# Kernel tuning notes

Measured on AMD Instinct MI355X. Metric: run time of the kernel, lower is better.

The kernel has to match this reference:

```python
import jax, jax.numpy as jnp
import numpy as np


def setup_inputs() -> dict:
    key = jax.random.key(0)
    kq, kk, kv = jax.random.split(key, 3)
    B, S, D = 4, 4096, 64
    return {
        "q": jax.random.normal(kq, (B, S, D), dtype=jnp.float32),
        "k": jax.random.normal(kk, (B, S, D), dtype=jnp.float32),
        "v": jax.random.normal(kv, (B, S, D), dtype=jnp.float32),
    }


def reference(q, k, v):
    B, S, D = q.shape
    scale = 1.0 / jnp.sqrt(jnp.asarray(D, dtype=q.dtype))
    # (B, S, S) full score matrix, as in the naive torch implementation
    scores = jnp.einsum("bqd,bkd->bqk", q, k) * scale
    causal_mask = jnp.tril(jnp.ones((S, S), dtype=bool))  # True = keep
    scores = jnp.where(causal_mask, scores, -jnp.inf)
    attn = jax.nn.softmax(scores, axis=-1)
    return jnp.einsum("bqk,bkd->bqd", attn, v)
```

## Files before the change

### kernel.cpp

```cpp
#include <hip/hip_runtime.h>
#include <hip/hip_bf16.h>

typedef __bf16 bf16x8 __attribute__((ext_vector_type(8)));
typedef __bf16 bf16x4 __attribute__((ext_vector_type(4)));
typedef float  floatx4 __attribute__((ext_vector_type(4)));

#define SD 4096
#define DH 64
#define NB 4

__device__ __forceinline__ float exp2fast(float x) { return __builtin_amdgcn_exp2f(x); }

__device__ __forceinline__ unsigned pack_bf16_2(float a, float b) {
    union { __bf16 h[2]; unsigned u; } cvt;
    cvt.h[0] = (__bf16)a; cvt.h[1] = (__bf16)b;
    return cvt.u;
}

__device__ __forceinline__ void sync_all() {
    asm volatile("s_waitcnt vmcnt(0) lgkmcnt(0)\n\ts_barrier" ::: "memory");
}

__device__ __forceinline__ void load_lds16(const void* g, void* l) {
    __builtin_amdgcn_global_load_lds(
        (const __attribute__((address_space(1))) unsigned int*)g,
        (__attribute__((address_space(3))) unsigned int*)l, 16, 0, 0);
}

__device__ __forceinline__ int swz8(int g) {
    int row = g >> 3, ch = g & 7;
    return row * 64 + ((ch ^ (row & 7)) << 3);
}

__global__ __launch_bounds__(256) void prep_kernel(const float* __restrict__ k,
                                                   const float* __restrict__ v,
                                                   __bf16* __restrict__ kbs,
                                                   __bf16* __restrict__ vts) {
    __shared__ __bf16 tile[64][72];
    const int bid = blockIdx.x;
    const int tid = threadIdx.x;
    const long base = (long)bid * 4096;

    {
        const float* src = k + base + tid * 16;
        float4 f0 = *(const float4*)(src);
        float4 f1 = *(const float4*)(src + 4);
        float4 f2 = *(const float4*)(src + 8);
        float4 f3 = *(const float4*)(src + 12);
        bf16x8 c0, c1;
        c0[0]=(__bf16)f0.x; c0[1]=(__bf16)f0.y; c0[2]=(__bf16)f0.z; c0[3]=(__bf16)f0.w;
        c0[4]=(__bf16)f1.x; c0[5]=(__bf16)f1.y; c0[6]=(__bf16)f1.z; c0[7]=(__bf16)f1.w;
        c1[0]=(__bf16)f2.x; c1[1]=(__bf16)f2.y; c1[2]=(__bf16)f2.z; c1[3]=(__bf16)f2.w;
        c1[4]=(__bf16)f3.x; c1[5]=(__bf16)f3.y; c1[6]=(__bf16)f3.z; c1[7]=(__bf16)f3.w;
        __bf16* dst = kbs + base;
        *(bf16x8*)(dst + swz8(tid * 2))     = c0;
        *(bf16x8*)(dst + swz8(tid * 2 + 1)) = c1;
    }
    {
        int r = tid >> 2, ds0 = (tid & 3) * 16;
#pragma unroll
        for (int i = 0; i < 4; ++i) {
            float4 f = *(const float4*)(v + base + r * 64 + ds0 + i * 4);
            tile[ds0 + i*4 + 0][r] = (__bf16)f.x;
            tile[ds0 + i*4 + 1][r] = (__bf16)f.y;
            tile[ds0 + i*4 + 2][r] = (__bf16)f.z;
            tile[ds0 + i*4 + 3][r] = (__bf16)f.w;
        }
    }
    __syncthreads();
    {
        __bf16* dst = vts + base;
#pragma unroll
        for (int h = 0; h < 2; ++h) {
            int qc = tid * 2 + h;
            int d = qc >> 3, c8 = (qc & 7) * 8;
            bf16x8 o;
#pragma unroll
            for (int i = 0; i < 8; ++i) {
                int col = c8 + i;
                int key = ((col >> 5) * 2 + ((col >> 2) & 1)) * 16
                        + ((col >> 3) & 3) * 4 + (col & 3);
                o[i] = tile[d][key];
            }
            *(bf16x8*)(dst + swz8(qc)) = o;
        }
    }
}

__global__ __launch_bounds__(256, 4) void fa_kernel(const float* __restrict__ q,
                                                    const __bf16* __restrict__ kbs,
                                                    const __bf16* __restrict__ vts,
                                                    __bf16* __restrict__ opart,
                                                    float* __restrict__ lpart) {
    __shared__ __bf16 smem[2][8192];

    const int tid  = threadIdx.x;
    const int wave = tid >> 6;
    const int lane = tid & 63;
    const int c    = lane & 15;
    const int quad = lane >> 4;
    const int bid   = blockIdx.x;
    const int batch = bid & 3;
    const int pr    = (bid >> 2) & 31;
    const int qr    = bid >> 7;
    const float sc = 0.125f * 1.4426950408889634f;

    const long offB = (long)batch * SD * DH;

    const int sw   = c & 7;
    const int off0 = ((quad ^ sw) << 3);
    const int off1 = (((quad + 4) ^ sw) << 3);
    const int rowc = c * 64;

    const long tileB = (long)batch * 64;

    auto stage = [&](int kt, int bufi) {
        const char* gsrc = (wave < 2)
            ? (const char*)(kbs + (tileB + kt) * 4096) + wave * 4096
            : (const char*)(vts + (tileB + kt) * 4096) + (wave - 2) * 4096;
        char* ldst = (char*)(&smem[bufi][0]) + wave * 4096;
#pragma unroll
        for (int i = 0; i < 4; ++i)
            load_lds16(gsrc + i * 1024 + lane * 16, ldst + i * 1024);
    };

    bf16x8 qA0, qA1, qB0, qB1;
    {
        const int T0 = pr, T1 = 63 - pr;
        const float* qp0 = q + offB + (long)(T0 * 64 + wave * 16 + c) * DH + quad * 8;
        const float* qp1 = q + offB + (long)(T1 * 64 + wave * 16 + c) * DH + quad * 8;
        float4 a0 = *(const float4*)(qp0);
        float4 a1 = *(const float4*)(qp0 + 4);
        float4 a2 = *(const float4*)(qp0 + 32);
        float4 a3 = *(const float4*)(qp0 + 36);
        float4 b0 = *(const float4*)(qp1);
        float4 b1 = *(const float4*)(qp1 + 4);
        float4 b2 = *(const float4*)(qp1 + 32);
        float4 b3 = *(const float4*)(qp1 + 36);
        qA0[0]=(__bf16)(a0.x*sc); qA0[1]=(__bf16)(a0.y*sc); qA0[2]=(__bf16)(a0.z*sc); qA0[3]=(__bf16)(a0.w*sc);
        qA0[4]=(__bf16)(a1.x*sc); qA0[5]=(__bf16)(a1.y*sc); qA0[6]=(__bf16)(a1.z*sc); qA0[7]=(__bf16)(a1.w*sc);
        qA1[0]=(__bf16)(a2.x*sc); qA1[1]=(__bf16)(a2.y*sc); qA1[2]=(__bf16)(a2.z*sc); qA1[3]=(__bf16)(a2.w*sc);
        qA1[4]=(__bf16)(a3.x*sc); qA1[5]=(__bf16)(a3.y*sc); qA1[6]=(__bf16)(a3.z*sc); qA1[7]=(__bf16)(a3.w*sc);
        qB0[0]=(__bf16)(b0.x*sc); qB0[1]=(__bf16)(b0.y*sc); qB0[2]=(__bf16)(b0.z*sc); qB0[3]=(__bf16)(b0.w*sc);
        qB0[4]=(__bf16)(b1.x*sc); qB0[5]=(__bf16)(b1.y*sc); qB0[6]=(__bf16)(b1.z*sc); qB0[7]=(__bf16)(b1.w*sc);
        qB1[0]=(__bf16)(b2.x*sc); qB1[1]=(__bf16)(b2.y*sc); qB1[2]=(__bf16)(b2.z*sc); qB1[3]=(__bf16)(b2.w*sc);
        qB1[4]=(__bf16)(b3.x*sc); qB1[5]=(__bf16)(b3.y*sc); qB1[6]=(__bf16)(b3.z*sc); qB1[7]=(__bf16)(b3.w*sc);
    }

#pragma unroll 1
    for (int ph = 0; ph < 2; ++ph) {
        const int T = ph ? 63 - pr : pr;
        const int myq = T * 64 + wave * 16;
        const int qrow = myq + c;

        const bf16x8 qf0 = ph ? qB0 : qA0;
        const bf16x8 qf1 = ph ? qB1 : qA1;

        floatx4 o0 = {0.f,0.f,0.f,0.f}, o1 = o0, o2 = o0, o3 = o0;
        float l = 0.0f;

        const int n = (T >= qr) ? ((T - qr) >> 3) + 1 : 0;

        sync_all();
        if (n > 0) stage(qr, 0);

#pragma unroll 1
        for (int j = 0; j < n; ++j) {
            const int kt = qr + 8 * j;
            sync_all();
            if (j + 1 < n) stage(kt + 8, (j + 1) & 1);

            const int kbase = kt * 64;
            if (kbase > myq + 15) continue;

            const __bf16* kbuf = &smem[j & 1][0];
            const __bf16* vbuf = kbuf + 4096;
            floatx4 sa[4];
            __builtin_amdgcn_s_setprio(1);
#pragma unroll
            for (int t = 0; t < 4; ++t) {
                bf16x8 ka  = *(const bf16x8*)(kbuf + t * 1024 + rowc + off0);
                bf16x8 kb2 = *(const bf16x8*)(kbuf + t * 1024 + rowc + off1);
                floatx4 a = {0.f,0.f,0.f,0.f};
                a = __builtin_amdgcn_mfma_f32_16x16x32_bf16(ka,  qf0, a, 0, 0, 0);
                a = __builtin_amdgcn_mfma_f32_16x16x32_bf16(kb2, qf1, a, 0, 0, 0);
                sa[t] = a;
            }
            __builtin_amdgcn_s_setprio(0);
            float pe[16];
            if (kbase + 63 > myq) {
#pragma unroll
                for (int t = 0; t < 4; ++t)
#pragma unroll
                    for (int r = 0; r < 4; ++r) {
                        int key = kbase + t*16 + quad*4 + r;
                        pe[t*4+r] = (key <= qrow) ? exp2fast(sa[t][r]) : 0.0f;
                    }
            } else {
#pragma unroll
                for (int t = 0; t < 4; ++t)
#pragma unroll
                    for (int r = 0; r < 4; ++r) pe[t*4+r] = exp2fast(sa[t][r]);
            }
            {
                float s8[8], s4v[4];
#pragma unroll
                for (int i = 0; i < 8; ++i) s8[i] = pe[i] + pe[i+8];
#pragma unroll
                for (int i = 0; i < 4; ++i) s4v[i] = s8[i] + s8[i+4];
                l += (s4v[0] + s4v[2]) + (s4v[1] + s4v[3]);
            }
            __builtin_amdgcn_s_setprio(1);
#pragma unroll
            for (int s = 0; s < 2; ++s) {
                union { unsigned u[4]; bf16x8 f; } bp;
#pragma unroll
                for (int jj = 0; jj < 4; ++jj)
                    bp.u[jj] = pack_bf16_2(pe[8*s + 2*jj], pe[8*s + 2*jj + 1]);
                const int offs = s ? off1 : off0;
                bf16x8 v0 = *(const bf16x8*)(vbuf + 0*1024 + rowc + offs);
                bf16x8 v1 = *(const bf16x8*)(vbuf + 1*1024 + rowc + offs);
                bf16x8 v2 = *(const bf16x8*)(vbuf + 2*1024 + rowc + offs);
                bf16x8 v3 = *(const bf16x8*)(vbuf + 3*1024 + rowc + offs);
                o0 = __builtin_amdgcn_mfma_f32_16x16x32_bf16(v0, bp.f, o0, 0, 0, 0);
                o1 = __builtin_amdgcn_mfma_f32_16x16x32_bf16(v1, bp.f, o1, 0, 0, 0);
                o2 = __builtin_amdgcn_mfma_f32_16x16x32_bf16(v2, bp.f, o2, 0, 0, 0);
                o3 = __builtin_amdgcn_mfma_f32_16x16x32_bf16(v3, bp.f, o3, 0, 0, 0);
            }
            __builtin_amdgcn_s_setprio(0);
        }

        l += __shfl_xor(l, 16);
        l += __shfl_xor(l, 32);

        if (n > 0) {
            __bf16* ob = opart + ((long)qr * NB + batch) * (long)(SD * DH) + (long)myq * DH;
            {
                floatx4 ov[4] = {o0, o1, o2, o3};
#pragma unroll
                for (int dt = 0; dt < 4; ++dt) {
                    uint2 sO;
                    sO.x = pack_bf16_2(ov[dt][0], ov[dt][1]);
                    sO.y = pack_bf16_2(ov[dt][2], ov[dt][3]);
                    *(uint2*)(ob + c * DH + dt*16 + quad*4) = sO;
                }
            }
            if (quad == 0)
                lpart[((long)qr * NB + batch) * SD + myq + c] = l;
        }
    }
}

__global__ __launch_bounds__(256) void combine_kernel(const __bf16* __restrict__ opart,
                                                      const float* __restrict__ lpart,
                                                      float* __restrict__ out) {
    const long t     = (long)blockIdx.x * 256 + threadIdx.x;
    const long base8 = t * 8;
    const long qq    = base8 >> 6;
    const int  T     = ((int)(qq & (SD - 1))) >> 6;
    const int  nqr   = (T < 7 ? T : 7) + 1;
    float a0=0.f,a1=0.f,a2=0.f,a3=0.f,a4=0.f,a5=0.f,a6=0.f,a7=0.f, den=0.f;
    for (int qr = 0; qr < nqr; ++qr) {
        bf16x8 p = *(const bf16x8*)(opart + ((long)qr << 20) + base8);
        a0 += (float)p[0]; a1 += (float)p[1]; a2 += (float)p[2]; a3 += (float)p[3];
        a4 += (float)p[4]; a5 += (float)p[5]; a6 += (float)p[6]; a7 += (float)p[7];
        den += lpart[((long)qr << 14) + qq];
    }
    const float inv = 1.0f / den;
    float4 o0, o1;
    o0.x = a0*inv; o0.y = a1*inv; o0.z = a2*inv; o0.w = a3*inv;
    o1.x = a4*inv; o1.y = a5*inv; o1.z = a6*inv; o1.w = a7*inv;
    *(float4*)(out + base8)     = o0;
    *(float4*)(out + base8 + 4) = o1;
}

extern "C" void kernel_launch(void* const* d_in, const int* in_sizes, int n_in,
                              void* d_out, int out_size, void* d_ws, size_t ws_size,
                              hipStream_t stream) {
    const float* q = (const float*)d_in[0];
    const float* k = (const float*)d_in[1];
    const float* v = (const float*)d_in[2];
    float* out = (float*)d_out;
    __bf16* kbs   = (__bf16*)d_ws;
    __bf16* vts   = (__bf16*)((char*)d_ws + (2u << 20));
    __bf16* opart = (__bf16*)((char*)d_ws + (4u << 20));
    float*  lpart = (float*)((char*)d_ws + (20u << 20));
    prep_kernel<<<dim3(256), dim3(256), 0, stream>>>(k, v, kbs, vts);
    fa_kernel<<<dim3(1024), dim3(256), 0, stream>>>(q, kbs, vts, opart, lpart);
    combine_kernel<<<dim3(512), dim3(256), 0, stream>>>(opart, lpart, out);
}
```

Measured before the change: 88.42 us.

## Double query rows per wave and widen key split to sixteen partitions

Each wave now processes 32 query rows (two 16-row MFMA tiles) against every staged K/V tile, so each LDS load of K and V feeds twice as many MFMAs. Query tiles grow to 128 rows with 16 pairs, and the key dimension is split into 16 strided partitions instead of 8, which keeps the grid at 1024 blocks. The combine kernel reads up to 16 partials per row, and the lpart workspace offset moves to make room for the larger opart buffer. This doubles the partial-output traffic and accumulator register use, which may lower occupancy, in exchange for better reuse of K/V fragments.

```diff
diff --git a/kernel.cpp b/kernel.cpp
--- a/kernel.cpp
+++ b/kernel.cpp
@@ -101,8 +101,8 @@
     const int quad = lane >> 4;
     const int bid   = blockIdx.x;
     const int batch = bid & 3;
-    const int pr    = (bid >> 2) & 31;
-    const int qr    = bid >> 7;
+    const int pr    = (bid >> 2) & 15;
+    const int qr    = bid >> 6;
     const float sc = 0.125f * 1.4426950408889634f;
 
     const long offB = (long)batch * SD * DH;
@@ -124,77 +124,78 @@
             load_lds16(gsrc + i * 1024 + lane * 16, ldst + i * 1024);
     };
 
-    bf16x8 qA0, qA1, qB0, qB1;
-    {
-        const int T0 = pr, T1 = 63 - pr;
-        const float* qp0 = q + offB + (long)(T0 * 64 + wave * 16 + c) * DH + quad * 8;
-        const float* qp1 = q + offB + (long)(T1 * 64 + wave * 16 + c) * DH + quad * 8;
-        float4 a0 = *(const float4*)(qp0);
-        float4 a1 = *(const float4*)(qp0 + 4);
-        float4 a2 = *(const float4*)(qp0 + 32);
-        float4 a3 = *(const float4*)(qp0 + 36);
-        float4 b0 = *(const float4*)(qp1);
-        float4 b1 = *(const float4*)(qp1 + 4);
-        float4 b2 = *(const float4*)(qp1 + 32);
-        float4 b3 = *(const float4*)(qp1 + 36);
-        qA0[0]=(__bf16)(a0.x*sc); qA0[1]=(__bf16)(a0.y*sc); qA0[2]=(__bf16)(a0.z*sc); qA0[3]=(__bf16)(a0.w*sc);
-        qA0[4]=(__bf16)(a1.x*sc); qA0[5]=(__bf16)(a1.y*sc); qA0[6]=(__bf16)(a1.z*sc); qA0[7]=(__bf16)(a1.w*sc);
-        qA1[0]=(__bf16)(a2.x*sc); qA1[1]=(__bf16)(a2.y*sc); qA1[2]=(__bf16)(a2.z*sc); qA1[3]=(__bf16)(a2.w*sc);
-        qA1[4]=(__bf16)(a3.x*sc); qA1[5]=(__bf16)(a3.y*sc); qA1[6]=(__bf16)(a3.z*sc); qA1[7]=(__bf16)(a3.w*sc);
-        qB0[0]=(__bf16)(b0.x*sc); qB0[1]=(__bf16)(b0.y*sc); qB0[2]=(__bf16)(b0.z*sc); qB0[3]=(__bf16)(b0.w*sc);
-        qB0[4]=(__bf16)(b1.x*sc); qB0[5]=(__bf16)(b1.y*sc); qB0[6]=(__bf16)(b1.z*sc); qB0[7]=(__bf16)(b1.w*sc);
-        qB1[0]=(__bf16)(b2.x*sc); qB1[1]=(__bf16)(b2.y*sc); qB1[2]=(__bf16)(b2.z*sc); qB1[3]=(__bf16)(b2.w*sc);
-        qB1[4]=(__bf16)(b3.x*sc); qB1[5]=(__bf16)(b3.y*sc); qB1[6]=(__bf16)(b3.z*sc); qB1[7]=(__bf16)(b3.w*sc);
-    }
-
 #pragma unroll 1
     for (int ph = 0; ph < 2; ++ph) {
-        const int T = ph ? 63 - pr : pr;
-        const int myq = T * 64 + wave * 16;
-        const int qrow = myq + c;
-
-        const bf16x8 qf0 = ph ? qB0 : qA0;
-        const bf16x8 qf1 = ph ? qB1 : qA1;
+        const int T = ph ? 31 - pr : pr;
+        const int myq = T * 128 + wave * 32;
+        const int TK = 2 * T + 1;
+
+        bf16x8 qf0, qf1, qf2, qf3;
+        {
+            const float* qp0 = q + offB + (long)(myq + c) * DH + quad * 8;
+            const float* qp1 = qp0 + 16 * DH;
+            float4 a0 = *(const float4*)(qp0);
+            float4 a1 = *(const float4*)(qp0 + 4);
+            float4 a2 = *(const float4*)(qp0 + 32);
+            float4 a3 = *(const float4*)(qp0 + 36);
+            float4 b0 = *(const float4*)(qp1);
+            float4 b1 = *(const float4*)(qp1 + 4);
+            float4 b2 = *(const float4*)(qp1 + 32);
+            float4 b3 = *(const float4*)(qp1 + 36);
+            qf0[0]=(__bf16)(a0.x*sc); qf0[1]=(__bf16)(a0.y*sc); qf0[2]=(__bf16)(a0.z*sc); qf0[3]=(__bf16)(a0.w*sc);
+            qf0[4]=(__bf16)(a1.x*sc); qf0[5]=(__bf16)(a1.y*sc); qf0[6]=(__bf16)(a1.z*sc); qf0[7]=(__bf16)(a1.w*sc);
+            qf1[0]=(__bf16)(a2.x*sc); qf1[1]=(__bf16)(a2.y*sc); qf1[2]=(__bf16)(a2.z*sc); qf1[3]=(__bf16)(a2.w*sc);
+            qf1[4]=(__bf16)(a3.x*sc); qf1[5]=(__bf16)(a3.y*sc); qf1[6]=(__bf16)(a3.z*sc); qf1[7]=(__bf16)(a3.w*sc);
+            qf2[0]=(__bf16)(b0.x*sc); qf2[1]=(__bf16)(b0.y*sc); qf2[2]=(__bf16)(b0.z*sc); qf2[3]=(__bf16)(b0.w*sc);
+            qf2[4]=(__bf16)(b1.x*sc); qf2[5]=(__bf16)(b1.y*sc); qf2[6]=(__bf16)(b1.z*sc); qf2[7]=(__bf16)(b1.w*sc);
+            qf3[0]=(__bf16)(b2.x*sc); qf3[1]=(__bf16)(b2.y*sc); qf3[2]=(__bf16)(b2.z*sc); qf3[3]=(__bf16)(b2.w*sc);
+            qf3[4]=(__bf16)(b3.x*sc); qf3[5]=(__bf16)(b3.y*sc); qf3[6]=(__bf16)(b3.z*sc); qf3[7]=(__bf16)(b3.w*sc);
+        }
 
         floatx4 o0 = {0.f,0.f,0.f,0.f}, o1 = o0, o2 = o0, o3 = o0;
-        float l = 0.0f;
-
-        const int n = (T >= qr) ? ((T - qr) >> 3) + 1 : 0;
+        floatx4 o4 = o0, o5 = o0, o6 = o0, o7 = o0;
+        float l0 = 0.0f, l1 = 0.0f;
+
+        const int n = (TK >= qr) ? ((TK - qr) >> 4) + 1 : 0;
 
         sync_all();
         if (n > 0) stage(qr, 0);
 
 #pragma unroll 1
         for (int j = 0; j < n; ++j) {
-            const int kt = qr + 8 * j;
+            const int kt = qr + 16 * j;
             sync_all();
-            if (j + 1 < n) stage(kt + 8, (j + 1) & 1);
+            if (j + 1 < n) stage(kt + 16, (j + 1) & 1);
 
             const int kbase = kt * 64;
-            if (kbase > myq + 15) continue;
+            if (kbase > myq + 31) continue;
 
             const __bf16* kbuf = &smem[j & 1][0];
             const __bf16* vbuf = kbuf + 4096;
-            floatx4 sa[4];
+            floatx4 sa[4], sb[4];
             __builtin_amdgcn_s_setprio(1);
 #pragma unroll
             for (int t = 0; t < 4; ++t) {
                 bf16x8 ka  = *(const bf16x8*)(kbuf + t * 1024 + rowc + off0);
                 bf16x8 kb2 = *(const bf16x8*)(kbuf + t * 1024 + rowc + off1);
                 floatx4 a = {0.f,0.f,0.f,0.f};
+                floatx4 b = {0.f,0.f,0.f,0.f};
                 a = __builtin_amdgcn_mfma_f32_16x16x32_bf16(ka,  qf0, a, 0, 0, 0);
                 a = __builtin_amdgcn_mfma_f32_16x16x32_bf16(kb2, qf1, a, 0, 0, 0);
-                sa[t] = a;
+                b = __builtin_amdgcn_mfma_f32_16x16x32_bf16(ka,  qf2, b, 0, 0, 0);
+                b = __builtin_amdgcn_mfma_f32_16x16x32_bf16(kb2, qf3, b, 0, 0, 0);
+                sa[t] = a; sb[t] = b;
             }
             __builtin_amdgcn_s_setprio(0);
-            float pe[16];
+            float pe[16], pf[16];
             if (kbase + 63 > myq) {
+                const int qrow0 = myq + c;
 #pragma unroll
                 for (int t = 0; t < 4; ++t)
 #pragma unroll
                     for (int r = 0; r < 4; ++r) {
                         int key = kbase + t*16 + quad*4 + r;
-                        pe[t*4+r] = (key <= qrow) ? exp2fast(sa[t][r]) : 0.0f;
+                        pe[t*4+r] = (key <= qrow0) ? exp2fast(sa[t][r]) : 0.0f;
                     }
             } else {
 #pragma unroll
@@ -202,21 +203,43 @@
 #pragma unroll
                     for (int r = 0; r < 4; ++r) pe[t*4+r] = exp2fast(sa[t][r]);
             }
+            if (kbase + 63 > myq + 16) {
+                const int qrow1 = myq + 16 + c;
+#pragma unroll
+                for (int t = 0; t < 4; ++t)
+#pragma unroll
+                    for (int r = 0; r < 4; ++r) {
+                        int key = kbase + t*16 + quad*4 + r;
+                        pf[t*4+r] = (key <= qrow1) ? exp2fast(sb[t][r]) : 0.0f;
+                    }
+            } else {
+#pragma unroll
+                for (int t = 0; t < 4; ++t)
+#pragma unroll
+                    for (int r = 0; r < 4; ++r) pf[t*4+r] = exp2fast(sb[t][r]);
+            }
             {
                 float s8[8], s4v[4];
 #pragma unroll
                 for (int i = 0; i < 8; ++i) s8[i] = pe[i] + pe[i+8];
 #pragma unroll
                 for (int i = 0; i < 4; ++i) s4v[i] = s8[i] + s8[i+4];
-                l += (s4v[0] + s4v[2]) + (s4v[1] + s4v[3]);
+                l0 += (s4v[0] + s4v[2]) + (s4v[1] + s4v[3]);
+#pragma unroll
+                for (int i = 0; i < 8; ++i) s8[i] = pf[i] + pf[i+8];
+#pragma unroll
+                for (int i = 0; i < 4; ++i) s4v[i] = s8[i] + s8[i+4];
+                l1 += (s4v[0] + s4v[2]) + (s4v[1] + s4v[3]);
             }
             __builtin_amdgcn_s_setprio(1);
 #pragma unroll
             for (int s = 0; s < 2; ++s) {
-                union { unsigned u[4]; bf16x8 f; } bp;
-#pragma unroll
-                for (int jj = 0; jj < 4; ++jj)
+                union { unsigned u[4]; bf16x8 f; } bp, bq;
+#pragma unroll
+                for (int jj = 0; jj < 4; ++jj) {
                     bp.u[jj] = pack_bf16_2(pe[8*s + 2*jj], pe[8*s + 2*jj + 1]);
+                    bq.u[jj] = pack_bf16_2(pf[8*s + 2*jj], pf[8*s + 2*jj + 1]);
+                }
                 const int offs = s ? off1 : off0;
                 bf16x8 v0 = *(const bf16x8*)(vbuf + 0*1024 + rowc + offs);
                 bf16x8 v1 = *(const bf16x8*)(vbuf + 1*1024 + rowc + offs);
@@ -226,12 +249,18 @@
                 o1 = __builtin_amdgcn_mfma_f32_16x16x32_bf16(v1, bp.f, o1, 0, 0, 0);
                 o2 = __builtin_amdgcn_mfma_f32_16x16x32_bf16(v2, bp.f, o2, 0, 0, 0);
                 o3 = __builtin_amdgcn_mfma_f32_16x16x32_bf16(v3, bp.f, o3, 0, 0, 0);
+                o4 = __builtin_amdgcn_mfma_f32_16x16x32_bf16(v0, bq.f, o4, 0, 0, 0);
+                o5 = __builtin_amdgcn_mfma_f32_16x16x32_bf16(v1, bq.f, o5, 0, 0, 0);
+                o6 = __builtin_amdgcn_mfma_f32_16x16x32_bf16(v2, bq.f, o6, 0, 0, 0);
+                o7 = __builtin_amdgcn_mfma_f32_16x16x32_bf16(v3, bq.f, o7, 0, 0, 0);
             }
             __builtin_amdgcn_s_setprio(0);
         }
 
-        l += __shfl_xor(l, 16);
-        l += __shfl_xor(l, 32);
+        l0 += __shfl_xor(l0, 16);
+        l0 += __shfl_xor(l0, 32);
+        l1 += __shfl_xor(l1, 16);
+        l1 += __shfl_xor(l1, 32);
 
         if (n > 0) {
             __bf16* ob = opart + ((long)qr * NB + batch) * (long)(SD * DH) + (long)myq * DH;
@@ -244,9 +273,19 @@
                     sO.y = pack_bf16_2(ov[dt][2], ov[dt][3]);
                     *(uint2*)(ob + c * DH + dt*16 + quad*4) = sO;
                 }
-            }
-            if (quad == 0)
-                lpart[((long)qr * NB + batch) * SD + myq + c] = l;
+                floatx4 ow[4] = {o4, o5, o6, o7};
+#pragma unroll
+                for (int dt = 0; dt < 4; ++dt) {
+                    uint2 sO;
+                    sO.x = pack_bf16_2(ow[dt][0], ow[dt][1]);
+                    sO.y = pack_bf16_2(ow[dt][2], ow[dt][3]);
+                    *(uint2*)(ob + (16 + c) * DH + dt*16 + quad*4) = sO;
+                }
+            }
+            if (quad == 0) {
+                lpart[((long)qr * NB + batch) * SD + myq + c]      = l0;
+                lpart[((long)qr * NB + batch) * SD + myq + 16 + c] = l1;
+            }
         }
     }
 }
@@ -257,8 +296,8 @@
     const long t     = (long)blockIdx.x * 256 + threadIdx.x;
     const long base8 = t * 8;
     const long qq    = base8 >> 6;
-    const int  T     = ((int)(qq & (SD - 1))) >> 6;
-    const int  nqr   = (T < 7 ? T : 7) + 1;
+    const int  TK    = (((int)(qq & (SD - 1))) >> 6) | 1;
+    const int  nqr   = (TK < 15 ? TK : 15) + 1;
     float a0=0.f,a1=0.f,a2=0.f,a3=0.f,a4=0.f,a5=0.f,a6=0.f,a7=0.f, den=0.f;
     for (int qr = 0; qr < nqr; ++qr) {
         bf16x8 p = *(const bf16x8*)(opart + ((long)qr << 20) + base8);
@@ -284,7 +323,7 @@
     __bf16* kbs   = (__bf16*)d_ws;
     __bf16* vts   = (__bf16*)((char*)d_ws + (2u << 20));
     __bf16* opart = (__bf16*)((char*)d_ws + (4u << 20));
-    float*  lpart = (float*)((char*)d_ws + (20u << 20));
+    float*  lpart = (float*)((char*)d_ws + (36u << 20));
     prep_kernel<<<dim3(256), dim3(256), 0, stream>>>(k, v, kbs, vts);
     fa_kernel<<<dim3(1024), dim3(256), 0, stream>>>(q, kbs, vts, opart, lpart);
     combine_kernel<<<dim3(512), dim3(256), 0, stream>>>(opart, lpart, out);
```

Measured after the change: 101.5 us. 1.15x slower.
